# Kernel tuning notes

Measured on AMD Instinct MI355X. Metric: run time of the kernel, lower is better.

## Reference

```python
import jax, jax.numpy as jnp
import numpy as np

H, DH, M, ITERS, DIM = 8, 64, 256, 6, 512
SCALE = DH ** -0.5


def setup_inputs() -> dict:
    key = jax.random.key(0)
    ks = jax.random.split(key, 6)
    b, n, nz = 4, 8192, 4096  # multiples of M=256 -> padding branch is a no-op
    s = DIM ** -0.5
    x = jax.random.normal(ks[0], (b, n, DIM), jnp.float32)
    z = jax.random.normal(ks[1], (b, nz, DIM), jnp.float32)
    W_q = jax.random.normal(ks[2], (DIM, H * DH), jnp.float32) * s      # to_qkv[0] (no bias)
    W_kv = jax.random.normal(ks[3], (DIM, 2 * H * DH), jnp.float32) * s  # to_qkv[1] (no bias)
    W_out = jax.random.normal(ks[4], (H * DH, DIM), jnp.float32) * s     # to_out Linear
    b_out = jax.random.normal(ks[5], (DIM,), jnp.float32) * 0.01
    return {"x": x, "z": z, "W_q": W_q, "W_kv": W_kv, "W_out": W_out, "b_out": b_out}


def moore_penrose_pinv(a, iters=ITERS):
    # Newton-Schulz iterative pseudo-inverse (faithful to moore_penrose_iter_pinv)
    abs_a = jnp.abs(a)
    col = abs_a.sum(axis=-1)
    row = abs_a.sum(axis=-2)
    zt = jnp.swapaxes(a, -1, -2) / (jnp.max(col) * jnp.max(row))
    I = jnp.eye(a.shape[-1], dtype=a.dtype)
    for _ in range(iters):
        az = a @ zt
        zt = 0.25 * zt @ (13.0 * I - az @ (15.0 * I - az @ (7.0 * I - az)))
    return zt


def reference(x, z, W_q, W_kv, W_out, b_out):
    b, n, _ = x.shape
    nz = z.shape[1]
    l, lz = n // M, nz // M  # landmark group sizes (n, nz are multiples of M)

    # projections (dropout=0.1 is inactive at inference; self.norm is never applied in forward)
    q = (x @ W_q).reshape(b, n, H, DH).transpose(0, 2, 1, 3) * SCALE   # [b,h,n,dh]
    kv = z @ W_kv
    k = kv[..., : H * DH].reshape(b, nz, H, DH).transpose(0, 2, 1, 3)  # [b,h,nz,dh]
    v = kv[..., H * DH :].reshape(b, nz, H, DH).transpose(0, 2, 1, 3)  # [b,h,nz,dh]

    # landmarks: mean over groups of l (resp. lz) consecutive tokens
    q_land = q.reshape(b, H, M, l, DH).sum(axis=3) / l    # [b,h,M,dh]
    k_land = k.reshape(b, H, M, lz, DH).sum(axis=3) / lz  # [b,h,M,dh]

    sim1 = jnp.einsum('bhid,bhjd->bhij', q, k_land)       # [b,h,n,M]
    sim2 = jnp.einsum('bhid,bhjd->bhij', q_land, k_land)  # [b,h,M,M]
    sim3 = jnp.einsum('bhid,bhjd->bhij', q_land, k)       # [b,h,M,nz]
    attn1 = jax.nn.softmax(sim1, axis=-1)
    attn2 = jax.nn.softmax(sim2, axis=-1)
    attn3 = jax.nn.softmax(sim3, axis=-1)

    attn2_inv = moore_penrose_pinv(attn2)
    # (attn1 @ attn2_inv) @ (attn3 @ v) computed small-first for efficiency; same math
    out = attn1 @ (attn2_inv @ (attn3 @ v))               # [b,h,n,dh]  (residual=False)

    out = out.transpose(0, 2, 1, 3).reshape(b, n, H * DH)
    out = out @ W_out + b_out
    return x + out
```

## Files before the change

### kernel.cpp

```cpp
#include <hip/hip_runtime.h>

typedef unsigned short u16;
typedef __attribute__((ext_vector_type(8))) short bf16x8s;
typedef __attribute__((ext_vector_type(4))) float f32x4;

#define DEV static __device__ __forceinline__

DEV float b2f(u16 v) { return __uint_as_float(((unsigned)v) << 16); }
DEV u16 f2b(float f) {
  unsigned u = __float_as_uint(f);
  unsigned r = (u + 0x7fffu + ((u >> 16) & 1u)) >> 16;
  return (u16)r;
}

#define GLL(gp, lp)                                                            \
  __builtin_amdgcn_global_load_lds(                                            \
      (const __attribute__((address_space(1))) unsigned int*)(gp),             \
      (__attribute__((address_space(3))) unsigned int*)(lp), 16, 0, 0)

#define MFMA __builtin_amdgcn_mfma_f32_16x16x32_bf16

__global__ __launch_bounds__(256) void k_f2b(const float* __restrict__ in,
                                             u16* __restrict__ o, long n4) {
  long i = (long)blockIdx.x * 256 + threadIdx.x;
  if (i >= n4) return;
  float4 v = *(const float4*)(in + i * 4);
  u16* d = o + i * 4;
  d[0] = f2b(v.x); d[1] = f2b(v.y); d[2] = f2b(v.z); d[3] = f2b(v.w);
}

__global__ __launch_bounds__(256) void k_wt(const float* __restrict__ W,
                                            u16* __restrict__ Wt, int N) {
  int e = blockIdx.x * 256 + threadIdx.x;
  int nn = e >> 9, kk = e & 511;
  Wt[e] = f2b(W[(long)kk * N + nn]);
}

template <int MODE>
__global__ __launch_bounds__(256, 2) void k_gemm128(
    const u16* __restrict__ A, const u16* __restrict__ Bm, void* __restrict__ C0,
    void* __restrict__ C1, const float* __restrict__ xres,
    const float* __restrict__ bias, int K) {
  const int nwg = gridDim.x * gridDim.y;
  const int orig = blockIdx.y * gridDim.x + blockIdx.x;
  const int qq = nwg >> 3, rr = nwg & 7;
  const int xcd = orig & 7, loc = orig >> 3;
  const int swz = (xcd < rr ? xcd * (qq + 1) : rr * (qq + 1) + (xcd - rr) * qq) + loc;
  const int m0 = (swz / gridDim.x) << 7, n0 = (swz % gridDim.x) << 7;
  const int t = threadIdx.x, lane = t & 63, w = t >> 6;
  const int wm = (w >> 1) << 6, wn = (w & 1) << 6;
  const int fr = lane & 15, g = lane >> 4;
  __shared__ u16 As[8192];
  __shared__ u16 Bs[8192];
  f32x4 acc[4][4] = {};
  const int srow = t >> 3, scs = t & 7;
  for (int k0 = 0; k0 < K; k0 += 64) {
    __syncthreads();
#pragma unroll
    for (int i = 0; i < 4; ++i) {
      int row = srow + (i << 5), cs = scs;
      GLL(A + (long)(m0 + row) * K + k0 + ((cs ^ (row & 7)) << 3),
          &As[(i << 11) + (w << 9)]);
      GLL(Bm + (long)(n0 + row) * K + k0 + ((cs ^ (row & 7)) << 3),
          &Bs[(i << 11) + (w << 9)]);
    }
    __syncthreads();
#pragma unroll
    for (int ks = 0; ks < 2; ++ks) {
      bf16x8s af[4], bf[4];
#pragma unroll
      for (int fi = 0; fi < 4; ++fi) {
        int row = wm + fi * 16 + fr;
        af[fi] = *(const bf16x8s*)((const char*)As + row * 128 +
                                   (((ks * 4 + g) ^ (row & 7)) << 4));
      }
#pragma unroll
      for (int fj = 0; fj < 4; ++fj) {
        int row = wn + fj * 16 + fr;
        bf[fj] = *(const bf16x8s*)((const char*)Bs + row * 128 +
                                   (((ks * 4 + g) ^ (row & 7)) << 4));
      }
#pragma unroll
      for (int fi = 0; fi < 4; ++fi)
#pragma unroll
        for (int fj = 0; fj < 4; ++fj)
          acc[fi][fj] = MFMA(af[fi], bf[fj], acc[fi][fj], 0, 0, 0);
    }
  }
  const int crow = g << 2;
#pragma unroll
  for (int fi = 0; fi < 4; ++fi)
#pragma unroll
    for (int fj = 0; fj < 4; ++fj)
#pragma unroll
      for (int r = 0; r < 4; ++r) {
        int row = m0 + wm + fi * 16 + crow + r;
        int col = n0 + wn + fj * 16 + fr;
        float v = acc[fi][fj][r];
        if (MODE == 0) {
          int b = row >> 13, n = row & 8191, h = col >> 6, dh = col & 63;
          ((u16*)C0)[((((long)(b * 8 + h)) << 13) + n) * 64 + dh] = f2b(v * 0.125f);
        } else if (MODE == 1) {
          int b = row >> 12, nz = row & 4095;
          if (col < 512) {
            int h = col >> 6, dh = col & 63;
            ((u16*)C0)[((((long)(b * 8 + h)) << 12) + nz) * 64 + dh] = f2b(v);
          } else {
            int c2 = col - 512, h = c2 >> 6, dh = c2 & 63;
            ((u16*)C1)[((((long)(b * 8 + h) * 64 + dh)) << 12) + nz] = f2b(v);
          }
        } else if (MODE == 2) {
          long idx = ((long)row << 9) + col;
          ((float*)C0)[idx] = v + xres[idx] + bias[col];
        }
      }
}

__global__ __launch_bounds__(256) void k_landmark(const u16* __restrict__ src,
                                                  u16* __restrict__ hi,
                                                  u16* __restrict__ lo, int ntok,
                                                  int l, float inv) {
  int pidx = blockIdx.x * 4 + (threadIdx.x >> 6);
  int d = threadIdx.x & 63;
  int bh = pidx >> 8, m = pidx & 255;
  const u16* s = src + ((long)bh * ntok + (long)m * l) * 64 + d;
  float sum = 0.f;
  for (int j = 0; j < l; ++j) sum += b2f(s[j * 64]);
  sum *= inv;
  long o = ((long)bh * 256 + m) * 64 + d;
  u16 h = f2b(sum);
  hi[o] = h;
  lo[o] = f2b(sum - b2f(h));
}

__global__ __launch_bounds__(256, 2) void k_sim2(
    const u16* __restrict__ qlh, const u16* __restrict__ qll,
    const u16* __restrict__ klh, const u16* __restrict__ kll,
    float* __restrict__ attn2, u16* __restrict__ aNhi, u16* __restrict__ aNlo) {
  const int rb = blockIdx.x, bh = blockIdx.y;
  const int t = threadIdx.x, lane = t & 63, w = t >> 6;
  const int fr = lane & 15, g = lane >> 4;
  __shared__ char lds[65536];
  {
    const u16* kh = klh + (long)bh * 16384;
    const u16* kl = kll + (long)bh * 16384;
    int srow8 = lane >> 3, cs7 = lane & 7;
#pragma unroll
    for (int i = 0; i < 8; ++i) {
      int slab = w * 8 + i;
      int krow = slab * 8 + srow8;
      GLL(kh + krow * 64 + ((cs7 ^ (krow & 7)) << 3), lds + slab * 1024);
      GLL(kl + krow * 64 + ((cs7 ^ (krow & 7)) << 3), lds + 32768 + slab * 1024);
    }
  }
  long qoff = ((long)bh * 256 + rb * 64 + w * 16 + fr) * 64;
  bf16x8s qh0 = *(const bf16x8s*)(qlh + qoff + g * 8);
  bf16x8s qh1 = *(const bf16x8s*)(qlh + qoff + 32 + g * 8);
  bf16x8s ql0 = *(const bf16x8s*)(qll + qoff + g * 8);
  bf16x8s ql1 = *(const bf16x8s*)(qll + qoff + 32 + g * 8);
  __syncthreads();
  f32x4 s[16];
#pragma unroll
  for (int c = 0; c < 16; ++c) {
    int j = (c << 4) + fr;
    int o0 = j * 128 + ((g ^ (j & 7)) << 4);
    int o1 = j * 128 + (((4 + g) ^ (j & 7)) << 4);
    bf16x8s kh0 = *(const bf16x8s*)(lds + o0);
    bf16x8s kh1 = *(const bf16x8s*)(lds + o1);
    bf16x8s kl0 = *(const bf16x8s*)(lds + 32768 + o0);
    bf16x8s kl1 = *(const bf16x8s*)(lds + 32768 + o1);
    f32x4 zz = {};
    zz = MFMA(qh0, kh0, zz, 0, 0, 0);
    zz = MFMA(qh1, kh1, zz, 0, 0, 0);
    zz = MFMA(qh0, kl0, zz, 0, 0, 0);
    zz = MFMA(qh1, kl1, zz, 0, 0, 0);
    zz = MFMA(ql0, kh0, zz, 0, 0, 0);
    zz = MFMA(ql1, kh1, zz, 0, 0, 0);
    s[c] = zz;
  }
  float li[4];
#pragma unroll
  for (int r = 0; r < 4; ++r) {
    float m = s[0][r];
#pragma unroll
    for (int c = 1; c < 16; ++c) m = fmaxf(m, s[c][r]);
    m = fmaxf(m, __shfl_xor(m, 1, 64));
    m = fmaxf(m, __shfl_xor(m, 2, 64));
    m = fmaxf(m, __shfl_xor(m, 4, 64));
    m = fmaxf(m, __shfl_xor(m, 8, 64));
    float l = 0.f;
#pragma unroll
    for (int c = 0; c < 16; ++c) {
      float e = __expf(s[c][r] - m);
      s[c][r] = e;
      l += e;
    }
    l += __shfl_xor(l, 1, 64);
    l += __shfl_xor(l, 2, 64);
    l += __shfl_xor(l, 4, 64);
    l += __shfl_xor(l, 8, 64);
    li[r] = 1.f / l;
  }
#pragma unroll
  for (int c = 0; c < 16; ++c)
#pragma unroll
    for (int r = 0; r < 4; ++r) {
      int row = rb * 64 + w * 16 + (g << 2) + r;
      int col = (c << 4) + fr;
      long idx = ((long)bh << 16) + ((long)row << 8) + col;
      float p = s[c][r] * li[r];
      attn2[idx] = p;
      u16 h = f2b(p);
      aNhi[idx] = h;
      aNlo[idx] = f2b(p - b2f(h));
    }
}

__global__ __launch_bounds__(256) void k_colmax(const float* __restrict__ attn2,
                                                unsigned* __restrict__ cmax) {
  int bh = blockIdx.x, j = threadIdx.x, lane = j & 63, w = j >> 6;
  const float* p = attn2 + ((long)bh << 16) + j;
  float s = 0.f;
  for (int m = 0; m < 256; ++m) s += p[m * 256];
  float mx = s;
  for (int o = 1; o < 64; o <<= 1) mx = fmaxf(mx, __shfl_xor(mx, o, 64));
  __shared__ float r1[4];
  if (lane == 0) r1[w] = mx;
  __syncthreads();
  if (j == 0) {
    mx = fmaxf(fmaxf(r1[0], r1[1]), fmaxf(r1[2], r1[3]));
    atomicMax(cmax, __float_as_uint(mx));
  }
}

__global__ __launch_bounds__(256, 2) void k_t1part(
    const u16* __restrict__ qlb, const u16* __restrict__ kb,
    const u16* __restrict__ vtb, float* __restrict__ opart,
    float* __restrict__ pm_, float* __restrict__ pl_) {
  int orig = blockIdx.x;
  int xcd = orig & 7, idx = orig >> 3;
  int p = xcd * 16 + (idx >> 2);
  int rb = idx & 3;
  int bh = p >> 2, kc = p & 3;
  const int t = threadIdx.x, lane = t & 63, w = t >> 6;
  const int fr = lane & 15, g = lane >> 4;
  __shared__ char lds[65536];
  const u16* qrow = qlb + ((long)bh * 256 + rb * 64 + w * 16 + fr) * 64;
  bf16x8s qa0 = *(const bf16x8s*)(qrow + g * 8);
  bf16x8s qa1 = *(const bf16x8s*)(qrow + 32 + g * 8);
  f32x4 o[4] = {};
  float m[4] = {-3e38f, -3e38f, -3e38f, -3e38f};
  float l[4] = {};
  const long kbase = (long)bh * 262144;
  for (int cc = 0; cc < 4; ++cc) {
    int c0 = kc * 1024 + cc * 256;
    __syncthreads();
#pragma unroll
    for (int i = 0; i < 8; ++i) {
      int seg = (i << 8) + t, row = seg >> 3, cs = seg & 7;
      GLL(kb + kbase + (long)(c0 + row) * 64 + ((cs ^ (row & 7)) << 3),
          lds + (i << 12) + (w << 10));
    }
#pragma unroll
    for (int i = 0; i < 8; ++i) {
      int seg = (i << 8) + t, row = seg >> 5, cs = seg & 31;
      GLL(vtb + kbase + (long)row * 4096 + c0 + ((cs ^ (row & 7)) << 3),
          lds + 32768 + (i << 12) + (w << 10));
    }
    __syncthreads();
    f32x4 s[16];
#pragma unroll
    for (int c = 0; c < 16; ++c) {
      int j = c * 16 + fr;
      bf16x8s b0 = *(const bf16x8s*)(lds + j * 128 + ((g ^ (j & 7)) << 4));
      bf16x8s b1 = *(const bf16x8s*)(lds + j * 128 + (((4 + g) ^ (j & 7)) << 4));
      f32x4 zz = {};
      zz = MFMA(qa0, b0, zz, 0, 0, 0);
      zz = MFMA(qa1, b1, zz, 0, 0, 0);
      s[c] = zz;
    }
    float sc[4];
#pragma unroll
    for (int r = 0; r < 4; ++r) {
      float pm = s[0][r];
#pragma unroll
      for (int c = 1; c < 16; ++c) pm = fmaxf(pm, s[c][r]);
      pm = fmaxf(pm, __shfl_xor(pm, 1, 64));
      pm = fmaxf(pm, __shfl_xor(pm, 2, 64));
      pm = fmaxf(pm, __shfl_xor(pm, 4, 64));
      pm = fmaxf(pm, __shfl_xor(pm, 8, 64));
      float mn = fmaxf(m[r], pm);
      sc[r] = __expf(m[r] - mn);
      m[r] = mn;
    }
#pragma unroll
    for (int r = 0; r < 4; ++r) {
      float su = 0.f;
#pragma unroll
      for (int c = 0; c < 16; ++c) {
        float e = __expf(s[c][r] - m[r]);
        s[c][r] = e;
        su += e;
      }
      su += __shfl_xor(su, 1, 64);
      su += __shfl_xor(su, 2, 64);
      su += __shfl_xor(su, 4, 64);
      su += __shfl_xor(su, 8, 64);
      l[r] = l[r] * sc[r] + su;
    }
#pragma unroll
    for (int d = 0; d < 4; ++d)
#pragma unroll
      for (int r = 0; r < 4; ++r) o[d][r] *= sc[r];
    __syncthreads();
#pragma unroll
    for (int c = 0; c < 16; ++c)
#pragma unroll
      for (int r = 0; r < 4; ++r) {
        int row = (w << 4) + (g << 2) + r;
        int byin = (c << 5) + (fr << 1);
        *(u16*)(lds + row * 512 + (byin ^ ((row & 7) << 4))) = f2b(s[c][r]);
      }
    asm volatile("s_waitcnt lgkmcnt(0)" ::: "memory");
    __builtin_amdgcn_sched_barrier(0);
#pragma unroll
    for (int ss = 0; ss < 8; ++ss) {
      int prow = (w << 4) + fr;
      bf16x8s ap = *(const bf16x8s*)(lds + prow * 512 +
                                     (((ss * 64) + (g << 4)) ^ ((prow & 7) << 4)));
#pragma unroll
      for (int d = 0; d < 4; ++d) {
        int dh = (d << 4) + fr;
        bf16x8s bv = *(const bf16x8s*)(lds + 32768 + dh * 512 +
                                       (((ss * 4 + g) ^ (dh & 7)) << 4));
        o[d] = MFMA(ap, bv, o[d], 0, 0, 0);
      }
    }
  }
  __syncthreads();
  float* lf = (float*)lds;
#pragma unroll
  for (int d = 0; d < 4; ++d)
#pragma unroll
    for (int r = 0; r < 4; ++r)
      lf[((w << 4) + (g << 2) + r) * 76 + (d << 4) + fr] = o[d][r];
  __syncthreads();
  const long pb = (long)(bh * 4 + kc) * 256 + rb * 64;
#pragma unroll
  for (int i = 0; i < 4; ++i) {
    int row = i * 16 + (t >> 4);
    int c4 = (t & 15) << 2;
    float4 v = *(const float4*)&lf[row * 76 + c4];
    *(float4*)&opart[(pb + row) * 64 + c4] = v;
  }
  if (fr == 0) {
#pragma unroll
    for (int r = 0; r < 4; ++r) {
      int lr = (w << 4) + (g << 2) + r;
      pm_[pb + lr] = m[r];
      pl_[pb + lr] = l[r];
    }
  }
}

__global__ __launch_bounds__(256) void k_t1merge(
    const float* __restrict__ opart, const float* __restrict__ pm_,
    const float* __restrict__ pl_, u16* __restrict__ T1thi,
    u16* __restrict__ T1tlo) {
  const int rb = blockIdx.x, bh = blockIdx.y;
  const int t = threadIdx.x;
#pragma unroll
  for (int rp = 0; rp < 4; ++rp) {
    int row = rb * 64 + rp * 16 + (t >> 4);
    int dh4 = (t & 15) << 2;
    float pmv[4], M = -3e38f;
#pragma unroll
    for (int i = 0; i < 4; ++i) {
      pmv[i] = pm_[(long)(bh * 4 + i) * 256 + row];
      M = fmaxf(M, pmv[i]);
    }
    float L = 0.f, wt[4];
#pragma unroll
    for (int i = 0; i < 4; ++i) {
      wt[i] = __expf(pmv[i] - M);
      L += pl_[(long)(bh * 4 + i) * 256 + row] * wt[i];
    }
    float4 acc = {0.f, 0.f, 0.f, 0.f};
#pragma unroll
    for (int i = 0; i < 4; ++i) {
      float4 v = *(const float4*)&opart[((long)(bh * 4 + i) * 256 + row) * 64 + dh4];
      acc.x += v.x * wt[i]; acc.y += v.y * wt[i];
      acc.z += v.z * wt[i]; acc.w += v.w * wt[i];
    }
    float invL = 1.f / L;
    float vv[4] = {acc.x * invL, acc.y * invL, acc.z * invL, acc.w * invL};
#pragma unroll
    for (int e = 0; e < 4; ++e) {
      int dh = dh4 + e;
      long idx = (long)bh * 16384 + (long)dh * 256 + row;
      u16 h = f2b(vv[e]);
      T1thi[idx] = h;
      T1tlo[idx] = f2b(vv[e] - b2f(h));
    }
  }
}

template <int NP>
__global__ __launch_bounds__(256) void k_nn_mfma(
    const u16* __restrict__ Ahi, const u16* __restrict__ Alo,
    const u16* __restrict__ Bthi, const u16* __restrict__ Btlo,
    u16* __restrict__ CNhi, u16* __restrict__ CNlo,
    u16* __restrict__ CThi, u16* __restrict__ CTlo,
    int Nc, float sab, float sa, float cdiag) {
  const int bz = blockIdx.z;
  const long offA = (long)bz << 16;
  const long offB = (long)bz * ((long)Nc << 8);
  const int m0 = blockIdx.y << 6, n0 = blockIdx.x << 6;
  const int t = threadIdx.x, lane = t & 63, w = t >> 6;
  const int wm = (w >> 1) << 5, wn = (w & 1) << 5;
  const int fr = lane & 15, g = lane >> 4;
  __shared__ u16 lds[16384];
  u16* LAh = lds;
  u16* LAl = lds + 4096;
  u16* LBh = lds + 8192;
  u16* LBl = lds + 12288;
  f32x4 acc[2][2] = {};
  const int srow8 = lane >> 3, cs = lane & 7;
  for (int k0 = 0; k0 < 256; k0 += 64) {
    __syncthreads();
#pragma unroll
    for (int j = 0; j < 2; ++j) {
      int slab = w * 2 + j;
      int row = slab * 8 + srow8;
      long asrc = offA + (long)(m0 + row) * 256 + k0 + ((cs ^ (row & 7)) << 3);
      long bsrc = offB + (long)(n0 + row) * 256 + k0 + ((cs ^ (row & 7)) << 3);
      GLL(Ahi + asrc, LAh + slab * 512);
      GLL(Bthi + bsrc, LBh + slab * 512);
      if (NP == 3) {
        GLL(Alo + asrc, LAl + slab * 512);
        GLL(Btlo + bsrc, LBl + slab * 512);
      }
    }
    __syncthreads();
#pragma unroll
    for (int ks = 0; ks < 2; ++ks) {
      const int ra0 = wm + fr, ra1 = wm + 16 + fr;
      const int rb0 = wn + fr, rb1 = wn + 16 + fr;
#define RD(base, row) \
  (*(const bf16x8s*)((const char*)(base) + (row) * 128 + (((ks * 4 + g) ^ ((row) & 7)) << 4)))
      bf16x8s ah0 = RD(LAh, ra0), ah1 = RD(LAh, ra1);
      bf16x8s bh0 = RD(LBh, rb0), bh1 = RD(LBh, rb1);
      acc[0][0] = MFMA(ah0, bh0, acc[0][0], 0, 0, 0);
      acc[0][1] = MFMA(ah0, bh1, acc[0][1], 0, 0, 0);
      acc[1][0] = MFMA(ah1, bh0, acc[1][0], 0, 0, 0);
      acc[1][1] = MFMA(ah1, bh1, acc[1][1], 0, 0, 0);
      if (NP == 3) {
        bf16x8s al0 = RD(LAl, ra0), al1 = RD(LAl, ra1);
        bf16x8s bl0 = RD(LBl, rb0), bl1 = RD(LBl, rb1);
        acc[0][0] = MFMA(ah0, bl0, acc[0][0], 0, 0, 0);
        acc[0][0] = MFMA(al0, bh0, acc[0][0], 0, 0, 0);
        acc[0][1] = MFMA(ah0, bl1, acc[0][1], 0, 0, 0);
        acc[0][1] = MFMA(al0, bh1, acc[0][1], 0, 0, 0);
        acc[1][0] = MFMA(ah1, bl0, acc[1][0], 0, 0, 0);
        acc[1][0] = MFMA(al1, bh0, acc[1][0], 0, 0, 0);
        acc[1][1] = MFMA(ah1, bl1, acc[1][1], 0, 0, 0);
        acc[1][1] = MFMA(al1, bh1, acc[1][1], 0, 0, 0);
      }
#undef RD
    }
  }
  const int crow = g << 2;
  const long offC = (long)bz * ((long)Nc << 8);
#pragma unroll
  for (int i = 0; i < 2; ++i)
#pragma unroll
    for (int j = 0; j < 2; ++j)
#pragma unroll
      for (int r = 0; r < 4; ++r) {
        int row = m0 + wm + i * 16 + crow + r;
        int col = n0 + wn + j * 16 + fr;
        float v = sab * acc[i][j][r];
        if (sa != 0.f) {
          long ai = offA + ((long)row << 8) + col;
          v += sa * (b2f(Ahi[ai]) + b2f(Alo[ai]));
        }
        if (row == col) v += cdiag;
        if (CNhi) {
          long ci = offC + (long)row * Nc + col;
          u16 h = f2b(v);
          if (CNlo) { CNhi[ci] = h; CNlo[ci] = f2b(v - b2f(h)); }
          else CNhi[ci] = h;
        }
        if (CThi) {
          long ti = offC + ((long)col << 8) + row;
          u16 h = f2b(v);
          CThi[ti] = h;
          if (CTlo) CTlo[ti] = f2b(v - b2f(h));
        }
      }
}

__global__ __launch_bounds__(256) void k_prep_pinv(
    const float* __restrict__ attn2, const unsigned* __restrict__ cmax,
    u16* __restrict__ zNhi, u16* __restrict__ zNlo,
    u16* __restrict__ zThi, u16* __restrict__ zTlo) {
  const int bz = blockIdx.z, i0 = blockIdx.y << 6, j0 = blockIdx.x << 6;
  const float s = 1.f / __uint_as_float(*cmax);
  const float* base = attn2 + ((long)bz << 16);
  __shared__ float mt[64][65];
  const int r = threadIdx.x >> 2, cb = (threadIdx.x & 3) << 4;
#pragma unroll
  for (int c4 = 0; c4 < 16; c4 += 4) {
    float4 v = *(const float4*)&base[(long)(j0 + r) * 256 + i0 + cb + c4];
    mt[r][cb + c4] = v.x; mt[r][cb + c4 + 1] = v.y;
    mt[r][cb + c4 + 2] = v.z; mt[r][cb + c4 + 3] = v.w;
  }
  __syncthreads();
  const int i = i0 + r;
#pragma unroll
  for (int c4 = 0; c4 < 16; c4 += 4) {
    float4 v = *(const float4*)&base[(long)i * 256 + j0 + cb + c4];
    float vv[4] = {v.x, v.y, v.z, v.w};
#pragma unroll
    for (int e = 0; e < 4; ++e) {
      int j = j0 + cb + c4 + e;
      long idx = ((long)bz << 16) + ((long)i << 8) + j;
      float zt = vv[e] * s;
      u16 zh = f2b(zt);
      zThi[idx] = zh; zTlo[idx] = f2b(zt - b2f(zh));
      float zn = mt[cb + c4 + e][r] * s;
      u16 nh = f2b(zn);
      zNhi[idx] = nh; zNlo[idx] = f2b(zn - b2f(nh));
    }
  }
}

__global__ __launch_bounds__(256) void k_fused_attn1(const u16* __restrict__ q,
                                                     const u16* __restrict__ klb,
                                                     const u16* __restrict__ t2t,
                                                     u16* __restrict__ O) {
  const int bh = blockIdx.y, n0 = blockIdx.x << 6;
  const int bb = bh >> 3, hh = bh & 7;
  const int t = threadIdx.x, lane = t & 63, w = t >> 6;
  const int fr = lane & 15, g = lane >> 4;
  __shared__ char lds[65536];
  {
    const u16* ks = klb + (long)bh * 16384;
    const u16* ts = t2t + (long)bh * 16384;
    int srow8 = lane >> 3, cs7 = lane & 7;
    int srow2 = lane >> 5, seg32 = lane & 31;
#pragma unroll
    for (int i = 0; i < 8; ++i) {
      int slab = w * 8 + i;
      int krow = slab * 8 + srow8;
      GLL(ks + krow * 64 + ((cs7 ^ (krow & 7)) << 3), lds + slab * 1024);
      int trow = slab * 2 + srow2;
      GLL(ts + trow * 256 + ((seg32 ^ (trow & 7)) << 3), lds + 32768 + slab * 1024);
    }
  }
  __syncthreads();
  const u16* qrow = q + ((long)bh * 8192 + n0 + (w << 4) + fr) * 64;
  bf16x8s qa0 = *(const bf16x8s*)(qrow + g * 8);
  bf16x8s qa1 = *(const bf16x8s*)(qrow + 32 + g * 8);
  f32x4 s[16];
#pragma unroll
  for (int c = 0; c < 16; ++c) {
    int j = (c << 4) + fr;
    bf16x8s b0 = *(const bf16x8s*)(lds + j * 128 + ((g ^ (j & 7)) << 4));
    bf16x8s b1 = *(const bf16x8s*)(lds + j * 128 + (((4 + g) ^ (j & 7)) << 4));
    f32x4 zz = {};
    zz = MFMA(qa0, b0, zz, 0, 0, 0);
    zz = MFMA(qa1, b1, zz, 0, 0, 0);
    s[c] = zz;
  }
  float li[4];
#pragma unroll
  for (int r = 0; r < 4; ++r) {
    float m = s[0][r];
#pragma unroll
    for (int c = 1; c < 16; ++c) m = fmaxf(m, s[c][r]);
    m = fmaxf(m, __shfl_xor(m, 1, 64));
    m = fmaxf(m, __shfl_xor(m, 2, 64));
    m = fmaxf(m, __shfl_xor(m, 4, 64));
    m = fmaxf(m, __shfl_xor(m, 8, 64));
    float l = 0.f;
#pragma unroll
    for (int c = 0; c < 16; ++c) {
      float e = __expf(s[c][r] - m);
      s[c][r] = e;
      l += e;
    }
    l += __shfl_xor(l, 1, 64);
    l += __shfl_xor(l, 2, 64);
    l += __shfl_xor(l, 4, 64);
    l += __shfl_xor(l, 8, 64);
    li[r] = 1.f / l;
  }
  __syncthreads();
#pragma unroll
  for (int c = 0; c < 16; ++c)
#pragma unroll
    for (int r = 0; r < 4; ++r) {
      int row = (w << 4) + (g << 2) + r;
      int byin = (c << 5) + (fr << 1);
      *(u16*)(lds + row * 512 + (byin ^ ((row & 7) << 4))) = f2b(s[c][r]);
    }
  asm volatile("s_waitcnt lgkmcnt(0)" ::: "memory");
  __builtin_amdgcn_sched_barrier(0);
  f32x4 o4[4] = {};
#pragma unroll
  for (int ss = 0; ss < 8; ++ss) {
    int prow = (w << 4) + fr;
    bf16x8s ap = *(const bf16x8s*)(lds + prow * 512 +
                                   (((ss * 64) + (g << 4)) ^ ((prow & 7) << 4)));
#pragma unroll
    for (int d = 0; d < 4; ++d) {
      int dh = (d << 4) + fr;
      bf16x8s bv = *(const bf16x8s*)(lds + 32768 + dh * 512 +
                                     (((ss * 4 + g) ^ (dh & 7)) << 4));
      o4[d] = MFMA(ap, bv, o4[d], 0, 0, 0);
    }
  }
  u16* ob = O + (((long)bb * 8192 + n0 + (w << 4)) << 9) + (hh << 6);
#pragma unroll
  for (int d = 0; d < 4; ++d)
#pragma unroll
    for (int r = 0; r < 4; ++r) {
      int row = (g << 2) + r;
      int col = (d << 4) + fr;
      ob[((long)row << 9) + col] = f2b(o4[d][r] * li[r]);
    }
}

extern "C" void kernel_launch(void* const* d_in, const int* in_sizes, int n_in,
                              void* d_out, int out_size, void* d_ws, size_t ws_size,
                              hipStream_t stream) {
  const float* x = (const float*)d_in[0];
  const float* z = (const float*)d_in[1];
  const float* Wq = (const float*)d_in[2];
  const float* Wkv = (const float*)d_in[3];
  const float* Wo = (const float*)d_in[4];
  const float* bo = (const float*)d_in[5];
  float* out = (float*)d_out;

  char* base = (char*)d_ws;
  size_t off = 0;
  auto alloc = [&](size_t bytes) -> void* {
    void* r = base + off;
    off = (off + bytes + 255) & ~(size_t)255;
    return r;
  };
  u16* qb = (u16*)alloc(33554432);
  u16* kb = (u16*)alloc(16777216);
  u16* vtb = (u16*)alloc(16777216);
  u16* PS = (u16*)alloc(67108864);
  float* attn2 = (float*)alloc(8388608);
  u16* xb = (u16*)alloc(33554432);
  u16* zb = (u16*)alloc(16777216);
  u16* wqt = (u16*)alloc(524288);
  u16* wkvt = (u16*)alloc(1048576);
  u16* wot = (u16*)alloc(524288);
  u16* qlh = (u16*)alloc(1048576);
  u16* qll = (u16*)alloc(1048576);
  u16* klh = (u16*)alloc(1048576);
  u16* kll = (u16*)alloc(1048576);
  u16* T1t = (u16*)alloc(2097152);
  u16* T2t = (u16*)alloc(1048576);
  unsigned* cmax = (unsigned*)alloc(256);
  const long MC = 2097152;
  u16* P = PS;
  u16 *ztA_Nhi = P,          *ztA_Nlo = P + MC,      *ztA_Thi = P + 2 * MC,  *ztA_Tlo = P + 3 * MC;
  u16 *ztB_Nhi = P + 4 * MC,  *ztB_Nlo = P + 5 * MC,  *ztB_Thi = P + 6 * MC,  *ztB_Tlo = P + 7 * MC;
  u16 *az_Nhi = P + 8 * MC,   *az_Nlo = P + 9 * MC,   *az_Thi = P + 10 * MC,  *az_Tlo = P + 11 * MC;
  u16 *taThi = P + 12 * MC,   *taTlo = P + 13 * MC;
  u16 *tcThi = P + 14 * MC,   *tcTlo = P + 15 * MC;
  u16 *aNhi = zb, *aNlo = zb + MC;
  float* opart = (float*)PS;
  float* pm_ = opart + 2097152;
  float* pl_ = pm_ + 32768;
  u16* T1thi = T1t;
  u16* T1tlo = T1t + 524288;
  u16* Ob = xb;

  hipMemsetAsync(cmax, 0, 4, stream);
  k_f2b<<<16384, 256, 0, stream>>>(x, xb, 4194304);
  k_f2b<<<8192, 256, 0, stream>>>(z, zb, 2097152);
  k_wt<<<1024, 256, 0, stream>>>(Wq, wqt, 512);
  k_wt<<<2048, 256, 0, stream>>>(Wkv, wkvt, 1024);
  k_wt<<<1024, 256, 0, stream>>>(Wo, wot, 512);

  k_gemm128<0><<<dim3(4, 256), 256, 0, stream>>>(xb, wqt, qb, nullptr, nullptr,
                                                 nullptr, 512);
  k_gemm128<1><<<dim3(8, 128), 256, 0, stream>>>(zb, wkvt, kb, vtb, nullptr,
                                                 nullptr, 512);
  k_landmark<<<2048, 256, 0, stream>>>(qb, qlh, qll, 8192, 32, 1.f / 32.f);
  k_landmark<<<2048, 256, 0, stream>>>(kb, klh, kll, 4096, 16, 1.f / 16.f);

  k_sim2<<<dim3(4, 32), 256, 0, stream>>>(qlh, qll, klh, kll, attn2, aNhi, aNlo);
  k_colmax<<<32, 256, 0, stream>>>(attn2, cmax);

  k_t1part<<<512, 256, 0, stream>>>(qlh, kb, vtb, opart, pm_, pl_);
  k_t1merge<<<dim3(4, 32), 256, 0, stream>>>(opart, pm_, pl_, T1thi, T1tlo);

  k_prep_pinv<<<dim3(4, 4, 32), 256, 0, stream>>>(attn2, cmax, ztA_Nhi, ztA_Nlo,
                                                  ztA_Thi, ztA_Tlo);

  dim3 g256(4, 4, 32);
  u16 *cN0 = ztA_Nhi, *cN1 = ztA_Nlo, *cT0 = ztA_Thi, *cT1 = ztA_Tlo;
  u16 *nN0 = ztB_Nhi, *nN1 = ztB_Nlo, *nT0 = ztB_Thi, *nT1 = ztB_Tlo;
  for (int it = 0; it < 6; ++it) {
    bool last = (it == 5);
    if (it < 3) {
      k_nn_mfma<1><<<g256, 256, 0, stream>>>(aNhi, aNlo, cT0, cT1, az_Nhi, az_Nlo,
                                             az_Thi, az_Tlo, 256, 1.f, 0.f, 0.f);
      k_nn_mfma<1><<<g256, 256, 0, stream>>>(az_Nhi, az_Nlo, az_Thi, az_Tlo, nullptr,
                                             nullptr, taThi, taTlo, 256, 1.f, -7.f, 15.f);
      k_nn_mfma<1><<<g256, 256, 0, stream>>>(az_Nhi, az_Nlo, taThi, taTlo, nullptr,
                                             nullptr, tcThi, tcTlo, 256, -1.f, 0.f, 13.f);
      k_nn_mfma<1><<<g256, 256, 0, stream>>>(cN0, cN1, tcThi, tcTlo, nN0, nN1,
                                             nT0, nT1, 256, 0.25f, 0.f, 0.f);
    } else {
      k_nn_mfma<3><<<g256, 256, 0, stream>>>(aNhi, aNlo, cT0, cT1, az_Nhi, az_Nlo,
                                             az_Thi, az_Tlo, 256, 1.f, 0.f, 0.f);
      k_nn_mfma<3><<<g256, 256, 0, stream>>>(az_Nhi, az_Nlo, az_Thi, az_Tlo, nullptr,
                                             nullptr, taThi, taTlo, 256, 1.f, -7.f, 15.f);
      k_nn_mfma<3><<<g256, 256, 0, stream>>>(az_Nhi, az_Nlo, taThi, taTlo, nullptr,
                                             nullptr, tcThi, tcTlo, 256, -1.f, 0.f, 13.f);
      k_nn_mfma<3><<<g256, 256, 0, stream>>>(cN0, cN1, tcThi, tcTlo, nN0, nN1,
                                             last ? nullptr : nT0, last ? nullptr : nT1,
                                             256, 0.25f, 0.f, 0.f);
    }
    u16* t0;
    t0 = cN0; cN0 = nN0; nN0 = t0;  t0 = cN1; cN1 = nN1; nN1 = t0;
    t0 = cT0; cT0 = nT0; nT0 = t0;  t0 = cT1; cT1 = nT1; nT1 = t0;
  }
  k_nn_mfma<3><<<dim3(1, 4, 32), 256, 0, stream>>>(cN0, cN1, T1thi, T1tlo, nullptr,
                                                   nullptr, T2t, nullptr, 64,
                                                   1.f, 0.f, 0.f);

  k_fused_attn1<<<dim3(128, 32), 256, 0, stream>>>(qb, klh, T2t, Ob);
  k_gemm128<2><<<dim3(4, 256), 256, 0, stream>>>(Ob, wot, out, nullptr, x, bo, 512);
}
```

Measured before the change: 664.4 us.

## Fuse Newton-Schulz pseudo-inverse chain into one cooperative persistent kernel

The pseudo-inverse stage was a chain of separate launches: a prep kernel, 24 small 256x256 matmul kernels and a final product. These are replaced by a single cooperative kernel of 512 blocks that runs every step in turn, with grid-wide syncs between dependent matmuls. The goal is to remove the launch overhead and the idle gaps between these many tiny kernels. In exchange, it depends on all 512 blocks being resident at once, which is why launch bounds is set to 2 blocks per CU. Each grid.sync has its own cost, and the tighter register budget could slow the matmul tiles.

```diff
diff --git a/kernel.cpp b/kernel.cpp
--- a/kernel.cpp
+++ b/kernel.cpp
@@ -1,4 +1,7 @@
 #include <hip/hip_runtime.h>
+#include <hip/hip_cooperative_groups.h>
+
+namespace cg = cooperative_groups;
 
 typedef unsigned short u16;
 typedef __attribute__((ext_vector_type(8))) short bf16x8s;
@@ -406,20 +409,15 @@
 }
 
 template <int NP>
-__global__ __launch_bounds__(256) void k_nn_mfma(
-    const u16* __restrict__ Ahi, const u16* __restrict__ Alo,
-    const u16* __restrict__ Bthi, const u16* __restrict__ Btlo,
-    u16* __restrict__ CNhi, u16* __restrict__ CNlo,
-    u16* __restrict__ CThi, u16* __restrict__ CTlo,
-    int Nc, float sab, float sa, float cdiag) {
-  const int bz = blockIdx.z;
+DEV void nn_tile(const u16* __restrict__ Ahi, const u16* __restrict__ Alo,
+                 const u16* __restrict__ Bthi, const u16* __restrict__ Btlo,
+                 u16* CNhi, u16* CNlo, u16* CThi, u16* CTlo, int Nc, float sab,
+                 float sa, float cdiag, int bz, int m0, int n0, u16* lds, int t) {
   const long offA = (long)bz << 16;
   const long offB = (long)bz * ((long)Nc << 8);
-  const int m0 = blockIdx.y << 6, n0 = blockIdx.x << 6;
-  const int t = threadIdx.x, lane = t & 63, w = t >> 6;
+  const int lane = t & 63, w = t >> 6;
   const int wm = (w >> 1) << 5, wn = (w & 1) << 5;
   const int fr = lane & 15, g = lane >> 4;
-  __shared__ u16 lds[16384];
   u16* LAh = lds;
   u16* LAl = lds + 4096;
   u16* LBh = lds + 8192;
@@ -500,39 +498,89 @@
       }
 }
 
-__global__ __launch_bounds__(256) void k_prep_pinv(
-    const float* __restrict__ attn2, const unsigned* __restrict__ cmax,
-    u16* __restrict__ zNhi, u16* __restrict__ zNlo,
-    u16* __restrict__ zThi, u16* __restrict__ zTlo) {
-  const int bz = blockIdx.z, i0 = blockIdx.y << 6, j0 = blockIdx.x << 6;
-  const float s = 1.f / __uint_as_float(*cmax);
-  const float* base = attn2 + ((long)bz << 16);
-  __shared__ float mt[64][65];
-  const int r = threadIdx.x >> 2, cb = (threadIdx.x & 3) << 4;
-#pragma unroll
-  for (int c4 = 0; c4 < 16; c4 += 4) {
-    float4 v = *(const float4*)&base[(long)(j0 + r) * 256 + i0 + cb + c4];
-    mt[r][cb + c4] = v.x; mt[r][cb + c4 + 1] = v.y;
-    mt[r][cb + c4 + 2] = v.z; mt[r][cb + c4 + 3] = v.w;
-  }
-  __syncthreads();
-  const int i = i0 + r;
-#pragma unroll
-  for (int c4 = 0; c4 < 16; c4 += 4) {
-    float4 v = *(const float4*)&base[(long)i * 256 + j0 + cb + c4];
-    float vv[4] = {v.x, v.y, v.z, v.w};
-#pragma unroll
-    for (int e = 0; e < 4; ++e) {
-      int j = j0 + cb + c4 + e;
-      long idx = ((long)bz << 16) + ((long)i << 8) + j;
-      float zt = vv[e] * s;
-      u16 zh = f2b(zt);
-      zThi[idx] = zh; zTlo[idx] = f2b(zt - b2f(zh));
-      float zn = mt[cb + c4 + e][r] * s;
-      u16 nh = f2b(zn);
-      zNhi[idx] = nh; zNlo[idx] = f2b(zn - b2f(nh));
-    }
-  }
+__global__ __launch_bounds__(256, 2) void k_pinv_coop(
+    const u16* __restrict__ aNhi, const u16* __restrict__ aNlo,
+    u16* __restrict__ PS, const float* __restrict__ attn2,
+    const unsigned* __restrict__ cmax, const u16* __restrict__ T1thi,
+    const u16* __restrict__ T1tlo, u16* __restrict__ T2t) {
+  __shared__ u16 lds[16384];
+  cg::grid_group grid = cg::this_grid();
+  const int bid = blockIdx.x;
+  const int bz = bid >> 4, ty = (bid >> 2) & 3, tx = bid & 3;
+  const int t = threadIdx.x;
+  const int m0 = ty << 6, n0 = tx << 6;
+  const long MC = 2097152;
+  u16 *zA_N0 = PS,           *zA_N1 = PS + MC,      *zA_T0 = PS + 2 * MC,  *zA_T1 = PS + 3 * MC;
+  u16 *zB_N0 = PS + 4 * MC,  *zB_N1 = PS + 5 * MC,  *zB_T0 = PS + 6 * MC,  *zB_T1 = PS + 7 * MC;
+  u16 *azN0 = PS + 8 * MC,   *azN1 = PS + 9 * MC,   *azT0 = PS + 10 * MC,  *azT1 = PS + 11 * MC;
+  u16 *taT0 = PS + 12 * MC,  *taT1 = PS + 13 * MC;
+  u16 *tcT0 = PS + 14 * MC,  *tcT1 = PS + 15 * MC;
+
+  {
+    const float s = 1.f / __uint_as_float(*cmax);
+    const float* basep = attn2 + ((long)bz << 16);
+    float* mt = (float*)lds;
+    const int r = t >> 2, cb = (t & 3) << 4;
+#pragma unroll
+    for (int c4 = 0; c4 < 16; c4 += 4) {
+      float4 v = *(const float4*)&basep[(long)(n0 + r) * 256 + m0 + cb + c4];
+      mt[r * 65 + cb + c4] = v.x; mt[r * 65 + cb + c4 + 1] = v.y;
+      mt[r * 65 + cb + c4 + 2] = v.z; mt[r * 65 + cb + c4 + 3] = v.w;
+    }
+    __syncthreads();
+    const int i = m0 + r;
+#pragma unroll
+    for (int c4 = 0; c4 < 16; c4 += 4) {
+      float4 v = *(const float4*)&basep[(long)i * 256 + n0 + cb + c4];
+      float vv[4] = {v.x, v.y, v.z, v.w};
+#pragma unroll
+      for (int e = 0; e < 4; ++e) {
+        int j = n0 + cb + c4 + e;
+        long idx = ((long)bz << 16) + ((long)i << 8) + j;
+        float zt = vv[e] * s;
+        u16 zh = f2b(zt);
+        zA_T0[idx] = zh; zA_T1[idx] = f2b(zt - b2f(zh));
+        float zn = mt[(cb + c4 + e) * 65 + r] * s;
+        u16 nh = f2b(zn);
+        zA_N0[idx] = nh; zA_N1[idx] = f2b(zn - b2f(nh));
+      }
+    }
+  }
+  grid.sync();
+
+  for (int it = 0; it < 6; ++it) {
+    u16 *cN0, *cN1, *cT0, *cT1, *nN0, *nN1, *nT0, *nT1;
+    if ((it & 1) == 0) {
+      cN0 = zA_N0; cN1 = zA_N1; cT0 = zA_T0; cT1 = zA_T1;
+      nN0 = zB_N0; nN1 = zB_N1; nT0 = zB_T0; nT1 = zB_T1;
+    } else {
+      cN0 = zB_N0; cN1 = zB_N1; cT0 = zB_T0; cT1 = zB_T1;
+      nN0 = zA_N0; nN1 = zA_N1; nT0 = zA_T0; nT1 = zA_T1;
+    }
+    if (it < 3) {
+      nn_tile<1>(aNhi, aNlo, cT0, cT1, azN0, azN1, azT0, azT1, 256, 1.f, 0.f, 0.f, bz, m0, n0, lds, t);
+      grid.sync();
+      nn_tile<1>(azN0, azN1, azT0, azT1, nullptr, nullptr, taT0, taT1, 256, 1.f, -7.f, 15.f, bz, m0, n0, lds, t);
+      grid.sync();
+      nn_tile<1>(azN0, azN1, taT0, taT1, nullptr, nullptr, tcT0, tcT1, 256, -1.f, 0.f, 13.f, bz, m0, n0, lds, t);
+      grid.sync();
+      nn_tile<1>(cN0, cN1, tcT0, tcT1, nN0, nN1, nT0, nT1, 256, 0.25f, 0.f, 0.f, bz, m0, n0, lds, t);
+      grid.sync();
+    } else {
+      nn_tile<3>(aNhi, aNlo, cT0, cT1, azN0, azN1, azT0, azT1, 256, 1.f, 0.f, 0.f, bz, m0, n0, lds, t);
+      grid.sync();
+      nn_tile<3>(azN0, azN1, azT0, azT1, nullptr, nullptr, taT0, taT1, 256, 1.f, -7.f, 15.f, bz, m0, n0, lds, t);
+      grid.sync();
+      nn_tile<3>(azN0, azN1, taT0, taT1, nullptr, nullptr, tcT0, tcT1, 256, -1.f, 0.f, 13.f, bz, m0, n0, lds, t);
+      grid.sync();
+      nn_tile<3>(cN0, cN1, tcT0, tcT1, nN0, nN1, (it == 5) ? nullptr : nT0,
+                 (it == 5) ? nullptr : nT1, 256, 0.25f, 0.f, 0.f, bz, m0, n0, lds, t);
+      grid.sync();
+    }
+  }
+  if (tx == 0)
+    nn_tile<3>(zA_N0, zA_N1, T1thi, T1tlo, nullptr, nullptr, T2t, nullptr, 64,
+               1.f, 0.f, 0.f, bz, m0, 0, lds, t);
 }
 
 __global__ __launch_bounds__(256) void k_fused_attn1(const u16* __restrict__ q,
@@ -668,12 +716,6 @@
   u16* T2t = (u16*)alloc(1048576);
   unsigned* cmax = (unsigned*)alloc(256);
   const long MC = 2097152;
-  u16* P = PS;
-  u16 *ztA_Nhi = P,          *ztA_Nlo = P + MC,      *ztA_Thi = P + 2 * MC,  *ztA_Tlo = P + 3 * MC;
-  u16 *ztB_Nhi = P + 4 * MC,  *ztB_Nlo = P + 5 * MC,  *ztB_Thi = P + 6 * MC,  *ztB_Tlo = P + 7 * MC;
-  u16 *az_Nhi = P + 8 * MC,   *az_Nlo = P + 9 * MC,   *az_Thi = P + 10 * MC,  *az_Tlo = P + 11 * MC;
-  u16 *taThi = P + 12 * MC,   *taTlo = P + 13 * MC;
-  u16 *tcThi = P + 14 * MC,   *tcTlo = P + 15 * MC;
   u16 *aNhi = zb, *aNlo = zb + MC;
   float* opart = (float*)PS;
   float* pm_ = opart + 2097152;
@@ -702,41 +744,14 @@
   k_t1part<<<512, 256, 0, stream>>>(qlh, kb, vtb, opart, pm_, pl_);
   k_t1merge<<<dim3(4, 32), 256, 0, stream>>>(opart, pm_, pl_, T1thi, T1tlo);
 
-  k_prep_pinv<<<dim3(4, 4, 32), 256, 0, stream>>>(attn2, cmax, ztA_Nhi, ztA_Nlo,
-                                                  ztA_Thi, ztA_Tlo);
-
-  dim3 g256(4, 4, 32);
-  u16 *cN0 = ztA_Nhi, *cN1 = ztA_Nlo, *cT0 = ztA_Thi, *cT1 = ztA_Tlo;
-  u16 *nN0 = ztB_Nhi, *nN1 = ztB_Nlo, *nT0 = ztB_Thi, *nT1 = ztB_Tlo;
-  for (int it = 0; it < 6; ++it) {
-    bool last = (it == 5);
-    if (it < 3) {
-      k_nn_mfma<1><<<g256, 256, 0, stream>>>(aNhi, aNlo, cT0, cT1, az_Nhi, az_Nlo,
-                                             az_Thi, az_Tlo, 256, 1.f, 0.f, 0.f);
-      k_nn_mfma<1><<<g256, 256, 0, stream>>>(az_Nhi, az_Nlo, az_Thi, az_Tlo, nullptr,
-                                             nullptr, taThi, taTlo, 256, 1.f, -7.f, 15.f);
-      k_nn_mfma<1><<<g256, 256, 0, stream>>>(az_Nhi, az_Nlo, taThi, taTlo, nullptr,
-                                             nullptr, tcThi, tcTlo, 256, -1.f, 0.f, 13.f);
-      k_nn_mfma<1><<<g256, 256, 0, stream>>>(cN0, cN1, tcThi, tcTlo, nN0, nN1,
-                                             nT0, nT1, 256, 0.25f, 0.f, 0.f);
-    } else {
-      k_nn_mfma<3><<<g256, 256, 0, stream>>>(aNhi, aNlo, cT0, cT1, az_Nhi, az_Nlo,
-                                             az_Thi, az_Tlo, 256, 1.f, 0.f, 0.f);
-      k_nn_mfma<3><<<g256, 256, 0, stream>>>(az_Nhi, az_Nlo, az_Thi, az_Tlo, nullptr,
-                                             nullptr, taThi, taTlo, 256, 1.f, -7.f, 15.f);
-      k_nn_mfma<3><<<g256, 256, 0, stream>>>(az_Nhi, az_Nlo, taThi, taTlo, nullptr,
-                                             nullptr, tcThi, tcTlo, 256, -1.f, 0.f, 13.f);
-      k_nn_mfma<3><<<g256, 256, 0, stream>>>(cN0, cN1, tcThi, tcTlo, nN0, nN1,
-                                             last ? nullptr : nT0, last ? nullptr : nT1,
-                                             256, 0.25f, 0.f, 0.f);
-    }
-    u16* t0;
-    t0 = cN0; cN0 = nN0; nN0 = t0;  t0 = cN1; cN1 = nN1; nN1 = t0;
-    t0 = cT0; cT0 = nT0; nT0 = t0;  t0 = cT1; cT1 = nT1; nT1 = t0;
-  }
-  k_nn_mfma<3><<<dim3(1, 4, 32), 256, 0, stream>>>(cN0, cN1, T1thi, T1tlo, nullptr,
-                                                   nullptr, T2t, nullptr, 64,
-                                                   1.f, 0.f, 0.f);
+  {
+    const u16* a0 = aNhi; const u16* a1 = aNlo;
+    u16* ps = PS; const float* at2 = attn2; const unsigned* cm = cmax;
+    const u16* t1h = T1thi; const u16* t1l = T1tlo; u16* t2 = T2t;
+    void* cargs[8] = {&a0, &a1, &ps, &at2, &cm, &t1h, &t1l, &t2};
+    hipLaunchCooperativeKernel((void*)k_pinv_coop, dim3(512), dim3(256), cargs,
+                               0, stream);
+  }
 
   k_fused_attn1<<<dim3(128, 32), 256, 0, stream>>>(qb, klh, T2t, Ob);
   k_gemm128<2><<<dim3(4, 256), 256, 0, stream>>>(Ob, wot, out, nullptr, x, bo, 512);
```

After: 2.579 ms. 288% more time.
